# Performance work log

Hardware: AMD Instinct MI355X
Metric: run time of the kernel (lower is better)

The kernel has to match this reference:

```python
import jax, jax.numpy as jnp
import numpy as np

B, S, D = 2, 2048, 1024
H, HD = 16, 64          # num_heads, head_dim
W = 16                  # window_size; band half-width = W // 2 = 8


def setup_inputs() -> dict:
    key = jax.random.key(0)
    ks = jax.random.split(key, 5)
    std = 0.02
    inp = {
        'hidden_states': jax.random.normal(ks[0], (B, S, D), dtype=jnp.float32),
        'Wq': jax.random.normal(ks[1], (D, D), dtype=jnp.float32) * std,
        'Wk': jax.random.normal(ks[2], (D, D), dtype=jnp.float32) * std,
        'Wv': jax.random.normal(ks[3], (D, D), dtype=jnp.float32) * std,
        'Wo': jax.random.normal(ks[4], (D, D), dtype=jnp.float32) * std,
        'bq': jnp.zeros((D,), dtype=jnp.float32),
        'bk': jnp.zeros((D,), dtype=jnp.float32),
        'bv': jnp.zeros((D,), dtype=jnp.float32),
        'bo': jnp.zeros((D,), dtype=jnp.float32),
    }
    return inp


def reference(hidden_states, Wq, bq, Wk, bk, Wv, bv, Wo, bo):
    # Projections (y = x @ W + b)
    q = hidden_states @ Wq + bq   # [B,S,D]
    k = hidden_states @ Wk + bk
    v = hidden_states @ Wv + bv
    # Split heads -> [B,H,S,HD]
    q = q.reshape(B, S, H, HD).transpose(0, 2, 1, 3)
    k = k.reshape(B, S, H, HD).transpose(0, 2, 1, 3)
    v = v.reshape(B, S, H, HD).transpose(0, 2, 1, 3)
    # Band mask: original fills scores for j in [i - W//2, i + W//2]
    idx = jnp.arange(S)
    band = jnp.abs(idx[:, None] - idx[None, :]) <= (W // 2)   # [S,S]
    scores = jnp.einsum('bhsd,bhtd->bhst', q, k) / jnp.sqrt(jnp.float32(HD))
    # Faithful to source: out-of-band entries stay 0.0 (NOT -inf),
    # and softmax runs over the FULL row, so exp(0)=1 contributions remain.
    scores = jnp.where(band[None, None], scores, 0.0)
    attn = jax.nn.softmax(scores, axis=-1)                    # [B,H,S,S]
    ctx = jnp.einsum('bhst,bhtd->bhsd', attn, v)              # [B,H,S,HD]
    ctx = ctx.transpose(0, 2, 1, 3).reshape(B, S, D)
    return ctx @ Wo + bo
```

## Files before the change

### kernel.cpp

```cpp
#include <hip/hip_runtime.h>
#include <hip/hip_bf16.h>
#include <cmath>

#define S_LEN 2048
#define DMODEL 1024
#define NH 16
#define HD_DIM 64

typedef __bf16 bf16;
typedef __bf16 bf16x2 __attribute__((ext_vector_type(2)));
typedef __bf16 bf16x8 __attribute__((ext_vector_type(8)));
typedef float f32x4 __attribute__((ext_vector_type(4)));

__global__ __launch_bounds__(256) void prep_all(const float* __restrict__ x,
                                                const float* __restrict__ Wq,
                                                const float* __restrict__ Wk,
                                                const float* __restrict__ Wv,
                                                const float* __restrict__ Wo,
                                                const float* __restrict__ bq,
                                                const float* __restrict__ bk,
                                                const float* __restrict__ bv,
                                                bf16* __restrict__ xb,
                                                bf16* __restrict__ wtall,
                                                bf16* __restrict__ wot,
                                                float* __restrict__ ball,
                                                float* __restrict__ vsm) {
    __shared__ float tile[64][65];
    const int bid = blockIdx.x;
    const int tid = threadIdx.x;
    if (bid < 2048) {
        int i = (bid * 256 + tid) * 8;
        float4 v0 = *(const float4*)(x + i);
        float4 v1 = *(const float4*)(x + i + 4);
        bf16x8 o;
        o[0] = (bf16)v0.x; o[1] = (bf16)v0.y; o[2] = (bf16)v0.z; o[3] = (bf16)v0.w;
        o[4] = (bf16)v1.x; o[5] = (bf16)v1.y; o[6] = (bf16)v1.z; o[7] = (bf16)v1.w;
        *(bf16x8*)(xb + i) = o;
    } else if (bid < 3072) {
        int t = bid - 2048;
        int z = t >> 8;
        t &= 255;
        const float* W = (z == 0) ? Wq : (z == 1) ? Wk : (z == 2) ? Wv : Wo;
        bf16* Wt = (z == 3) ? wot : wtall + (size_t)z * 1048576;
        int n0 = (t & 15) * 64, k0 = (t >> 4) * 64;
        int tr = tid >> 6, tc = tid & 63;
#pragma unroll
        for (int i = 0; i < 16; ++i) {
            int r = tr + i * 4;
            tile[r][tc] = W[(size_t)(k0 + r) * DMODEL + n0 + tc];
        }
        __syncthreads();
#pragma unroll
        for (int i = 0; i < 16; ++i) {
            int r = tr + i * 4;
            Wt[(size_t)(n0 + r) * DMODEL + k0 + tc] = (bf16)tile[tc][r];
        }
    } else {
        int i = (bid - 3072) * 256 + tid;
        float v = (i < 1024) ? bq[i] : (i < 2048) ? bk[i - 1024] : bv[i - 2048];
        ball[i] = v;
        if (i >= 2048) {
            int c = i - 2048;
            vsm[c]        = 2048.0f * v;
            vsm[1024 + c] = 2048.0f * v;
        }
    }
}

__device__ __forceinline__ void gload_lds16(const void* g, void* l) {
    __builtin_amdgcn_global_load_lds((const __attribute__((address_space(1))) void*)g,
                                     (__attribute__((address_space(3))) void*)l, 16, 0, 0);
}

#define BAR() asm volatile("s_barrier" ::: "memory")
#define VMC(N) asm volatile("s_waitcnt vmcnt(" #N ")" ::: "memory")

#define QST(T, D) do {                                                                 \
    _Pragma("unroll") for (int _p = 0; _p < 4; ++_p)                                   \
        gload_lds16(aSrc + (size_t)(32 * _p) * KDIM + (size_t)(T) * 64,                \
                    aDstW + (D) * 16384 + _p * 4096);                                  \
    _Pragma("unroll") for (int _p = 0; _p < 6; ++_p)                                   \
        gload_lds16(bSrc + (size_t)(32 * _p) * KDIM + (size_t)(T) * 64,                \
                    bDstW + (D) * 24576 + _p * 4096);                                  \
} while (0)

template <int KDIM>
__global__ __launch_bounds__(256, 2) void gemm_qkv(const bf16* __restrict__ A,
                                                   const bf16* __restrict__ Bt,
                                                   bf16* __restrict__ C,
                                                   const float* __restrict__ bias,
                                                   float* __restrict__ vsm,
                                                   int N) {
    __shared__ bf16 smem[40960];
    char* sc = (char*)smem;

    const int tid  = threadIdx.x;
    const int wv   = tid >> 6;
    const int lane = tid & 63;
    const int ll   = lane & 15;
    const int kh   = lane >> 4;
    const int wm   = wv >> 1;
    const int wn   = wv & 1;

    const int flat = blockIdx.y * 32 + blockIdx.x;
    const int L    = (flat & 7) * 64 + (flat >> 3);
    const int m0   = (L & 31) * 128;
    const int n0   = (L >> 5) * 192;

    const int swcol = (((tid & 7) ^ ((tid >> 3) & 7)) << 3);
    const bf16* aSrc = A + (size_t)(m0 + (tid >> 3)) * KDIM + swcol;
    const bf16* bSrc = Bt + (size_t)(n0 + (tid >> 3)) * KDIM + swcol;
    char* aDstW = sc + wv * 1024;
    char* bDstW = sc + 32768 + wv * 1024;

    const int aBase = wm * 8192 + ll * 128;
    const int bBase = (wn * 96 + ll) * 128;
    const int ks0 = ((kh ^ (ll & 7)) << 4);
    const int ks1 = (((4 | kh) ^ (ll & 7)) << 4);

    f32x4 acc[4][6] = {};

    constexpr int NT = KDIM / 64;

    QST(0, 0);
    VMC(0); BAR();

#pragma unroll 1
    for (int t = 0; t < NT; ++t) {
        const int d = t & 1;
        if (t + 1 < NT) QST(t + 1, d ^ 1);

        bf16x8 a[4][2], b[3][2];
#pragma unroll
        for (int mf = 0; mf < 4; ++mf) {
            a[mf][0] = *(const bf16x8*)(sc + d * 16384 + aBase + mf * 2048 + ks0);
            a[mf][1] = *(const bf16x8*)(sc + d * 16384 + aBase + mf * 2048 + ks1);
        }
#pragma unroll
        for (int nf = 0; nf < 3; ++nf) {
            b[nf][0] = *(const bf16x8*)(sc + 32768 + d * 24576 + bBase + nf * 2048 + ks0);
            b[nf][1] = *(const bf16x8*)(sc + 32768 + d * 24576 + bBase + nf * 2048 + ks1);
        }
        __builtin_amdgcn_s_setprio(1);
#pragma unroll
        for (int mf = 0; mf < 4; ++mf)
#pragma unroll
            for (int nf = 0; nf < 3; ++nf)
#pragma unroll
                for (int k = 0; k < 2; ++k)
                    acc[mf][nf] = __builtin_amdgcn_mfma_f32_16x16x32_bf16(
                        a[mf][k], b[nf][k], acc[mf][nf], 0, 0, 0);
        __builtin_amdgcn_s_setprio(0);
#pragma unroll
        for (int nf = 0; nf < 3; ++nf) {
            b[nf][0] = *(const bf16x8*)(sc + 32768 + d * 24576 + bBase + (nf + 3) * 2048 + ks0);
            b[nf][1] = *(const bf16x8*)(sc + 32768 + d * 24576 + bBase + (nf + 3) * 2048 + ks1);
        }
        __builtin_amdgcn_s_setprio(1);
#pragma unroll
        for (int mf = 0; mf < 4; ++mf)
#pragma unroll
            for (int nf = 0; nf < 3; ++nf)
#pragma unroll
                for (int k = 0; k < 2; ++k)
                    acc[mf][nf + 3] = __builtin_amdgcn_mfma_f32_16x16x32_bf16(
                        a[mf][k], b[nf][k], acc[mf][nf + 3], 0, 0, 0);
        __builtin_amdgcn_s_setprio(0);

        VMC(0); BAR();
    }

#pragma unroll
    for (int nf = 0; nf < 6; ++nf) {
        const int col = n0 + wn * 96 + nf * 16 + ll;
        const float bv_ = bias[col];
#pragma unroll
        for (int mf = 0; mf < 4; ++mf) {
            const int row = m0 + wm * 64 + mf * 16 + kh * 4;
#pragma unroll
            for (int r = 0; r < 4; ++r)
                C[(size_t)(row + r) * N + col] = (bf16)(acc[mf][nf][r] + bv_);
        }
    }

    {
        const int bidx = m0 >> 11;
#pragma unroll
        for (int nf = 0; nf < 6; ++nf) {
            if (n0 + wn * 96 + nf * 16 >= 2048) {
                float p = 0.f;
#pragma unroll
                for (int mf = 0; mf < 4; ++mf)
#pragma unroll
                    for (int r = 0; r < 4; ++r) p += acc[mf][nf][r];
                p += __shfl_xor(p, 16);
                p += __shfl_xor(p, 32);
                if (kh == 0)
                    atomicAdd(vsm + bidx * 1024 + (n0 + wn * 96 + nf * 16 + ll - 2048), p);
            }
        }
    }
}

__global__ __launch_bounds__(256) void gemm_bt(const bf16* __restrict__ A,
                                               const bf16* __restrict__ Bt,
                                               float* __restrict__ C,
                                               const float* __restrict__ bias,
                                               int N, int K) {
    __shared__ bf16 As[64 * 32];
    __shared__ bf16 Bs[128 * 32];
    const int tid  = threadIdx.x;
    const int wave = tid >> 6;
    const int lane = tid & 63;

    const int flat = blockIdx.y * 64 + blockIdx.x;
    const int L    = (flat & 7) * 64 + (flat >> 3);
    const int m0   = (L & 63) * 64;
    const int n0   = (L >> 6) * 128;

    const int wm = (wave >> 1) * 32;
    const int wn = (wave & 1) * 64;
    const int lrow = lane & 15;
    const int kh   = lane >> 4;
    const int srow = tid >> 2;
    const int scol = (tid & 3) * 16;

    f32x4 acc[2][4] = {};

    for (int k0 = 0; k0 < K; k0 += 32) {
        {
            const char* ga = (const char*)(A + (size_t)(m0 + srow) * K + k0) + scol;
            gload_lds16(ga, (char*)As + wave * 1024);
#pragma unroll
            for (int p = 0; p < 2; ++p) {
                const char* gb = (const char*)(Bt + (size_t)(n0 + p * 64 + srow) * K + k0) + scol;
                gload_lds16(gb, (char*)Bs + p * 4096 + wave * 1024);
            }
        }
        __syncthreads();
        bf16x8 af[2], bfr[4];
#pragma unroll
        for (int mf = 0; mf < 2; ++mf)
            af[mf] = *(const bf16x8*)&As[(wm + mf * 16 + lrow) * 32 + kh * 8];
#pragma unroll
        for (int nf = 0; nf < 4; ++nf)
            bfr[nf] = *(const bf16x8*)&Bs[(wn + nf * 16 + lrow) * 32 + kh * 8];
#pragma unroll
        for (int mf = 0; mf < 2; ++mf)
#pragma unroll
            for (int nf = 0; nf < 4; ++nf)
                acc[mf][nf] = __builtin_amdgcn_mfma_f32_16x16x32_bf16(af[mf], bfr[nf], acc[mf][nf], 0, 0, 0);
        __syncthreads();
    }

#pragma unroll
    for (int mf = 0; mf < 2; ++mf) {
#pragma unroll
        for (int nf = 0; nf < 4; ++nf) {
            int col = n0 + wn + nf * 16 + lrow;
            float bv_ = bias[col];
#pragma unroll
            for (int r = 0; r < 4; ++r) {
                int row = m0 + wm + mf * 16 + kh * 4 + r;
                C[(size_t)row * N + col] = acc[mf][nf][r] + bv_;
            }
        }
    }
}

__global__ __launch_bounds__(256) void band_attn(const bf16* __restrict__ qkv,
                                                 const float* __restrict__ vsum,
                                                 bf16* __restrict__ ctx) {
    int bid = blockIdx.x;
    int it = bid & 31;
    int h  = (bid >> 5) & 15;
    int b  = bid >> 9;
    const int i0 = it * 64;

    __shared__ bf16 qs[64 * 72];
    __shared__ bf16 ks[80 * 72];
    __shared__ bf16 vs[80 * 72];
    __shared__ float wsc[64 * 19];
    __shared__ float wsum[64];

    int tid = threadIdx.x;

    for (int idx = tid; idx < 64 * 8; idx += 256) {
        int r = idx >> 3, c = idx & 7;
        size_t g = (size_t)(b * S_LEN + i0 + r) * 3072 + h * 64 + c * 8;
        *(int4*)&qs[r * 72 + c * 8] = *(const int4*)&qkv[g];
    }
    for (int idx = tid; idx < 80 * 8; idx += 256) {
        int r = idx >> 3, c = idx & 7;
        int j = i0 - 8 + r;
        int4 kv = {0, 0, 0, 0}, vv = {0, 0, 0, 0};
        if (j >= 0 && j < S_LEN) {
            size_t base = (size_t)(b * S_LEN + j) * 3072 + h * 64 + c * 8;
            kv = *(const int4*)&qkv[base + 1024];
            vv = *(const int4*)&qkv[base + 2048];
        }
        *(int4*)&ks[r * 72 + c * 8] = kv;
        *(int4*)&vs[r * 72 + c * 8] = vv;
    }
    __syncthreads();

    {
        int i = tid >> 2, jg = tid & 3;
        bf16x8 qv[8];
#pragma unroll
        for (int c = 0; c < 8; ++c) qv[c] = *(const bf16x8*)&qs[i * 72 + c * 8];
        for (int jj = jg; jj < 17; jj += 4) {
            int j = i0 + i - 8 + jj;
            float w = 0.f;
            if (j >= 0 && j < S_LEN) {
                float dot = 0.f;
#pragma unroll
                for (int c = 0; c < 8; ++c) {
                    bf16x8 kv = *(const bf16x8*)&ks[(i + jj) * 72 + c * 8];
#pragma unroll
                    for (int e = 0; e < 8; ++e) dot += (float)qv[c][e] * (float)kv[e];
                }
                w = expm1f(dot * 0.125f);
            }
            wsc[i * 19 + jj] = w;
        }
    }
    __syncthreads();
    if (tid < 64) {
        float s = 0.f;
#pragma unroll
        for (int jj = 0; jj < 17; ++jj) s += wsc[tid * 19 + jj];
        wsum[tid] = s + (float)S_LEN;
    }
    __syncthreads();

    {
        int d0 = (tid & 31) * 2, ig = tid >> 5;
        float vb0 = vsum[(b * NH + h) * HD_DIM + d0];
        float vb1 = vsum[(b * NH + h) * HD_DIM + d0 + 1];
        for (int i = ig; i < 64; i += 8) {
            float a0 = vb0, a1 = vb1;
#pragma unroll
            for (int jj = 0; jj < 17; ++jj) {
                float w = wsc[i * 19 + jj];
                bf16x2 pv = *(const bf16x2*)&vs[(i + jj) * 72 + d0];
                a0 += w * (float)pv[0];
                a1 += w * (float)pv[1];
            }
            float inv = 1.0f / wsum[i];
            bf16x2 st;
            st[0] = (bf16)(a0 * inv);
            st[1] = (bf16)(a1 * inv);
            *(bf16x2*)&ctx[(size_t)(b * S_LEN + i0 + i) * 1024 + h * 64 + d0] = st;
        }
    }
}

extern "C" void kernel_launch(void* const* d_in, const int* in_sizes, int n_in,
                              void* d_out, int out_size, void* d_ws, size_t ws_size,
                              hipStream_t stream) {
    const float* x  = (const float*)d_in[0];
    const float* Wq = (const float*)d_in[1];
    const float* Wk = (const float*)d_in[2];
    const float* Wv = (const float*)d_in[3];
    const float* Wo = (const float*)d_in[4];
    const float* bq = (const float*)d_in[5];
    const float* bk = (const float*)d_in[6];
    const float* bv = (const float*)d_in[7];
    const float* bo = (const float*)d_in[8];

    char* ws = (char*)d_ws;
    bf16*  xb    = (bf16*)(ws);
    bf16*  wtall = (bf16*)(ws + 8388608);
    bf16*  wot   = (bf16*)(ws + 14680064);
    float* ball  = (float*)(ws + 16777216);
    bf16*  qkv   = (bf16*)(ws + 16789504);
    bf16*  ctxb  = (bf16*)(ws + 41955328);
    float* vsm   = (float*)(ws + 50343936);

    prep_all<<<3084, 256, 0, stream>>>(x, Wq, Wk, Wv, Wo, bq, bk, bv,
                                       xb, wtall, wot, ball, vsm);

    gemm_qkv<1024><<<dim3(32, 16), 256, 0, stream>>>(xb, wtall, qkv, ball, vsm, 3072);

    band_attn<<<1024, 256, 0, stream>>>(qkv, vsm, ctxb);

    gemm_bt<<<dim3(64, 8), 256, 0, stream>>>(ctxb, wot, (float*)d_out, bo, 1024, 1024);
}
```

Measured before the change: 80.49 us.

## Double-buffer output-projection GEMM with swizzled LDS and BK=64, remap QKV tiles

Rewrites the output projection GEMM to use a 64-wide K step with double-buffered, XOR-swizzled LDS tiles. The next tile's global-to-LDS loads are issued before computing on the current one, replacing two barriers per 32-wide K step with a single wait and barrier per 64-wide step. It also raises MFMA priority and sets occupancy to 2 blocks per SM. Separately, it changes the block-to-tile mapping in the QKV GEMM so neighbouring blocks pair N tiles, aiming for better L2 reuse. The cost is more shared memory per block (48KB), which may limit occupancy.

```diff
diff --git a/kernel.cpp b/kernel.cpp
--- a/kernel.cpp
+++ b/kernel.cpp
@@ -104,8 +104,8 @@
 
     const int flat = blockIdx.y * 32 + blockIdx.x;
     const int L    = (flat & 7) * 64 + (flat >> 3);
-    const int m0   = (L & 31) * 128;
-    const int n0   = (L >> 5) * 192;
+    const int m0   = ((L & 63) >> 1) * 128;
+    const int n0   = ((L >> 6) * 2 + (L & 1)) * 192;
 
     const int swcol = (((tid & 7) ^ ((tid >> 3) & 7)) << 3);
     const bf16* aSrc = A + (size_t)(m0 + (tid >> 3)) * KDIM + swcol;
@@ -202,66 +202,92 @@
     }
 }
 
-__global__ __launch_bounds__(256) void gemm_bt(const bf16* __restrict__ A,
-                                               const bf16* __restrict__ Bt,
-                                               float* __restrict__ C,
-                                               const float* __restrict__ bias,
-                                               int N, int K) {
-    __shared__ bf16 As[64 * 32];
-    __shared__ bf16 Bs[128 * 32];
+#define OST(T, D) do {                                                                 \
+    _Pragma("unroll") for (int _p = 0; _p < 2; ++_p)                                   \
+        gload_lds16(aSrc + (size_t)(32 * _p) * 1024 + (size_t)(T) * 64,                \
+                    aDstW + (D) * 8192 + _p * 4096);                                   \
+    _Pragma("unroll") for (int _p = 0; _p < 4; ++_p)                                   \
+        gload_lds16(bSrc + (size_t)(32 * _p) * 1024 + (size_t)(T) * 64,                \
+                    bDstW + (D) * 16384 + _p * 4096);                                  \
+} while (0)
+
+__global__ __launch_bounds__(256, 2) void gemm_bt(const bf16* __restrict__ A,
+                                                  const bf16* __restrict__ Bt,
+                                                  float* __restrict__ C,
+                                                  const float* __restrict__ bias,
+                                                  int N, int K) {
+    __shared__ bf16 smem[24576];
+    char* sc = (char*)smem;
     const int tid  = threadIdx.x;
-    const int wave = tid >> 6;
+    const int wv   = tid >> 6;
     const int lane = tid & 63;
+    const int ll   = lane & 15;
+    const int kh   = lane >> 4;
+    const int wm   = wv >> 1;
+    const int wn   = wv & 1;
 
     const int flat = blockIdx.y * 64 + blockIdx.x;
     const int L    = (flat & 7) * 64 + (flat >> 3);
     const int m0   = (L & 63) * 64;
     const int n0   = (L >> 6) * 128;
 
-    const int wm = (wave >> 1) * 32;
-    const int wn = (wave & 1) * 64;
-    const int lrow = lane & 15;
-    const int kh   = lane >> 4;
-    const int srow = tid >> 2;
-    const int scol = (tid & 3) * 16;
+    const int swcol = (((tid & 7) ^ ((tid >> 3) & 7)) << 3);
+    const bf16* aSrc = A + (size_t)(m0 + (tid >> 3)) * 1024 + swcol;
+    const bf16* bSrc = Bt + (size_t)(n0 + (tid >> 3)) * 1024 + swcol;
+    char* aDstW = sc + wv * 1024;
+    char* bDstW = sc + 16384 + wv * 1024;
+
+    const int aBase = wm * 4096 + ll * 128;
+    const int bBase = (wn * 64 + ll) * 128;
+    const int ks0 = ((kh ^ (ll & 7)) << 4);
+    const int ks1 = (((4 | kh) ^ (ll & 7)) << 4);
 
     f32x4 acc[2][4] = {};
-
-    for (int k0 = 0; k0 < K; k0 += 32) {
-        {
-            const char* ga = (const char*)(A + (size_t)(m0 + srow) * K + k0) + scol;
-            gload_lds16(ga, (char*)As + wave * 1024);
-#pragma unroll
-            for (int p = 0; p < 2; ++p) {
-                const char* gb = (const char*)(Bt + (size_t)(n0 + p * 64 + srow) * K + k0) + scol;
-                gload_lds16(gb, (char*)Bs + p * 4096 + wave * 1024);
-            }
-        }
-        __syncthreads();
-        bf16x8 af[2], bfr[4];
+    const int NT = K / 64;
+
+    OST(0, 0);
+    VMC(0); BAR();
+
+#pragma unroll 1
+    for (int t = 0; t < NT; ++t) {
+        const int d = t & 1;
+        if (t + 1 < NT) OST(t + 1, d ^ 1);
+
+        bf16x8 a[2][2], b[4][2];
+#pragma unroll
+        for (int mf = 0; mf < 2; ++mf) {
+            a[mf][0] = *(const bf16x8*)(sc + d * 8192 + aBase + mf * 2048 + ks0);
+            a[mf][1] = *(const bf16x8*)(sc + d * 8192 + aBase + mf * 2048 + ks1);
+        }
+#pragma unroll
+        for (int nf = 0; nf < 4; ++nf) {
+            b[nf][0] = *(const bf16x8*)(sc + 16384 + d * 16384 + bBase + nf * 2048 + ks0);
+            b[nf][1] = *(const bf16x8*)(sc + 16384 + d * 16384 + bBase + nf * 2048 + ks1);
+        }
+
+        __builtin_amdgcn_s_setprio(1);
 #pragma unroll
         for (int mf = 0; mf < 2; ++mf)
-            af[mf] = *(const bf16x8*)&As[(wm + mf * 16 + lrow) * 32 + kh * 8];
-#pragma unroll
-        for (int nf = 0; nf < 4; ++nf)
-            bfr[nf] = *(const bf16x8*)&Bs[(wn + nf * 16 + lrow) * 32 + kh * 8];
-#pragma unroll
-        for (int mf = 0; mf < 2; ++mf)
 #pragma unroll
             for (int nf = 0; nf < 4; ++nf)
-                acc[mf][nf] = __builtin_amdgcn_mfma_f32_16x16x32_bf16(af[mf], bfr[nf], acc[mf][nf], 0, 0, 0);
-        __syncthreads();
+#pragma unroll
+                for (int k = 0; k < 2; ++k)
+                    acc[mf][nf] = __builtin_amdgcn_mfma_f32_16x16x32_bf16(
+                        a[mf][k], b[nf][k], acc[mf][nf], 0, 0, 0);
+        __builtin_amdgcn_s_setprio(0);
+
+        VMC(0); BAR();
     }
 
 #pragma unroll
     for (int mf = 0; mf < 2; ++mf) {
 #pragma unroll
         for (int nf = 0; nf < 4; ++nf) {
-            int col = n0 + wn + nf * 16 + lrow;
+            int col = n0 + wn * 64 + nf * 16 + ll;
             float bv_ = bias[col];
 #pragma unroll
             for (int r = 0; r < 4; ++r) {
-                int row = m0 + wm + mf * 16 + kh * 4 + r;
+                int row = m0 + wm * 32 + mf * 16 + kh * 4 + r;
                 C[(size_t)row * N + col] = acc[mf][nf][r] + bv_;
             }
         }
```

After: 72.53 us. 1.11x faster.
